# Performance work log

Hardware: AMD Instinct MI355X
Metric: run time of the kernel (lower is better)

The kernel has to match this reference:

```python
import jax, jax.numpy as jnp
import numpy as np

TEMP = 10.0  # self.temp in the module


def _l2norm(x, eps):
    # matches torch cosine_similarity / F.normalize eps-clamped L2 normalization
    n = jnp.sqrt(jnp.sum(x * x, axis=-1, keepdims=True))
    return x / jnp.maximum(n, eps)


def setup_inputs() -> dict:
    key = jax.random.key(0)
    k1, k2, k3, k4 = jax.random.split(key, 4)
    b, n, k, q, t, c = 2, 5, 5, 75, 196, 384  # 5-way 5-shot, 15 queries/way, ViT-S tokens
    return {
        "feat_shot": jax.random.normal(k1, (b, n, k, t, c), jnp.float32),
        "feat_query": jax.random.normal(k2, (b, q, t, c), jnp.float32),
        "x_shot": jax.random.normal(k3, (b, n, k, c), jnp.float32),
        "x_query": jax.random.normal(k4, (b, q, c), jnp.float32),
    }


def reference(feat_shot, feat_query, x_shot, x_query):
    b, n, k, t, c = feat_shot.shape
    # --- token-level cosine similarity branch ---
    fq = _l2norm(feat_query, 1e-8)                      # [b,q,t,c]
    fs = _l2norm(feat_shot.reshape(b, n, k * t, c), 1e-8)  # [b,n,k*t,c]
    # cosine sim of every query token vs every shot token of each class
    sim = jnp.einsum('bqtc,bnsc->bqnts', fq, fs)        # [b,q,n,t,k*t]
    # topk(k=1) over shot tokens -> max; .mean(-1) over the size-1 topk dim is identity;
    # then mean over query tokens t
    logits = jnp.max(sim, axis=-1).mean(axis=-1)        # [b,q,n]
    # --- global-feature classifier branch ---
    proto = _l2norm(x_shot.mean(axis=-2), 1e-12)        # prototype mean over k shots: [b,n,c]
    xq = _l2norm(x_query, 1e-12)                        # [b,q,c]
    cls_logits = TEMP * jnp.einsum('bqc,bnc->bqn', xq, proto)  # [b,q,n]
    return (logits, cls_logits)
```

## Files before the change

kernel.cpp:

```cpp
#include <hip/hip_runtime.h>
#include <hip/hip_bf16.h>
#include <hip/hip_fp8.h>
#include <stdint.h>


typedef __attribute__((ext_vector_type(8))) int int8v;
typedef __attribute__((ext_vector_type(4))) float f32x4;

__device__ __forceinline__ unsigned enc_f(float f) {
    unsigned b = __float_as_uint(f);
    return (b & 0x80000000u) ? ~b : (b | 0x80000000u);
}
__device__ __forceinline__ float dec_f(unsigned u) {
    unsigned b = (u & 0x80000000u) ? (u & 0x7FFFFFFFu) : ~u;
    return __uint_as_float(b);
}

__device__ __forceinline__ unsigned pack4_fp8(float a, float b, float c, float d) {
    int r = __builtin_amdgcn_cvt_pk_fp8_f32(a, b, 0, false);
    r = __builtin_amdgcn_cvt_pk_fp8_f32(c, d, r, true);
    return (unsigned)r;
}

__global__ void prep_kernel(const float* __restrict__ feat_query,
                            const float* __restrict__ feat_shot,
                            const float* __restrict__ x_shot,
                            unsigned* __restrict__ fqn,
                            unsigned* __restrict__ fsnp,
                            float* __restrict__ proto,
                            unsigned* __restrict__ P) {
    const int blk  = blockIdx.x;
    const int tid  = threadIdx.x;
    const int lane = tid & 63;
    const int wv   = tid >> 6;

    if (blk < 2478) {
        const int tr  = blk * 16 + wv * 4 + (lane >> 4);
        const int l16 = lane & 15;
        if (tr >= 39640) return;

        const float* row;
        unsigned* o32;
        bool zero = false;
        bool shot = false;
        if (tr < 29400) {
            row = feat_query + (size_t)tr * 384;
            o32 = fqn + (size_t)tr * 96;
        } else {
            const int sp = tr - 29400;
            const int bn = sp >> 10;
            const int s  = sp & 1023;
            row  = feat_shot + ((size_t)bn * 980 + s) * 384;
            zero = (s >= 980);
            shot = true;
            const int shh   = s >> 9;
            const int c     = s & 511;
            const int chunk = c >> 5;
            const int cl    = c & 31;
            o32 = fsnp + (size_t)bn * 98304 + shh * 49152 + chunk * 3072
                       + (cl >> 4) * 512 + (cl & 15) * 4;
        }
        int idxs[6];
#pragma unroll
        for (int j = 0; j < 6; ++j)
            idxs[j] = shot ? ((j >> 1) * 1024 + ((l16 >> 2) & 1) * 256
                              + (((j & 1) << 1) + (l16 >> 3)) * 64 + (l16 & 3))
                           : (l16 + 16 * j);

        if (zero) {
#pragma unroll
            for (int j = 0; j < 6; ++j) o32[idxs[j]] = 0u;
            return;
        }
        const float4* rf4 = (const float4*)row;
        float4 v[6];
        float ss = 0.f;
#pragma unroll
        for (int j = 0; j < 6; ++j) {
            v[j] = rf4[l16 + 16 * j];
            ss += v[j].x * v[j].x + v[j].y * v[j].y + v[j].z * v[j].z + v[j].w * v[j].w;
        }
#pragma unroll
        for (int off = 1; off < 16; off <<= 1) ss += __shfl_xor(ss, off, 64);
        const float sc = 1.0f / fmaxf(sqrtf(ss), 1e-8f);
#pragma unroll
        for (int j = 0; j < 6; ++j)
            o32[idxs[j]] = pack4_fp8(v[j].x * sc, v[j].y * sc, v[j].z * sc, v[j].w * sc);
    } else if (blk < 2481) {
        const int gw = (blk - 2478) * 4 + wv;
        if (gw >= 10) return;
        const float* base = x_shot + (size_t)gw * 5 * 384;
        float v[6];
        float ss = 0.f;
#pragma unroll
        for (int j = 0; j < 6; ++j) {
            float s = 0.f;
#pragma unroll
            for (int kk = 0; kk < 5; ++kk) s += base[kk * 384 + lane + 64 * j];
            s *= 0.2f;
            v[j] = s;
            ss += s * s;
        }
#pragma unroll
        for (int off = 1; off < 64; off <<= 1) ss += __shfl_xor(ss, off, 64);
        const float scale = 1.0f / fmaxf(sqrtf(ss), 1e-12f);
#pragma unroll
        for (int j = 0; j < 6; ++j) proto[(size_t)gw * 384 + lane + 64 * j] = v[j] * scale;
    } else {
        const int i = (blk - 2481) * 256 + tid;
        if (i < 147000) P[i] = 0u;
    }
}

__global__ __launch_bounds__(256, 2) void gemm_kernel(const uint8_t* __restrict__ fqn,
                                                      const uint8_t* __restrict__ fsnp,
                                                      unsigned* __restrict__ P) {
    const int p   = blockIdx.x;
    const int w   = (p & 7) * 145 + (p >> 3);
    const int b   = w / 580;
    const int rem = w - b * 580;
    const int mt  = rem / 10;
    const int g   = rem - mt * 10;
    const int sh  = g & 1;
    const int bc  = b * 5 + (g >> 1);
    const int m0  = mt * 256;

    const int tid  = threadIdx.x;
    const int lane = tid & 63;
    const int wv   = tid >> 6;
    const int l15  = lane & 15;
    const int hi   = lane >> 4;

    const uint8_t* Ag = fqn  + (size_t)b * 14700 * 384;
    const uint8_t* Bg = fsnp + (size_t)bc * 393216 + (size_t)sh * 196608;
    const uint8_t* bp = Bg + lane * 16;

    int8v A[4][3];
#pragma unroll
    for (int mi = 0; mi < 4; ++mi) {
        int row = m0 + wv * 64 + mi * 16 + l15;
        row = row < 14700 ? row : 14699;
        const uint8_t* pa = Ag + (size_t)row * 384 + hi * 32;
#pragma unroll
        for (int ks = 0; ks < 3; ++ks) {
            const uint4 x = *(const uint4*)(pa + ks * 128);
            const uint4 y = *(const uint4*)(pa + ks * 128 + 16);
            A[mi][ks] = (int8v){(int)x.x, (int)x.y, (int)x.z, (int)x.w,
                                (int)y.x, (int)y.y, (int)y.z, (int)y.w};
        }
    }

    float rmax[4][4];
#pragma unroll
    for (int mi = 0; mi < 4; ++mi)
#pragma unroll
        for (int i = 0; i < 4; ++i) rmax[mi][i] = -3.0e38f;

    uint4 S[3][4];
#pragma unroll
    for (int ks = 0; ks < 3; ++ks) {
        const uint8_t* p2 = bp + (size_t)ks * 4096;
#pragma unroll
        for (int j = 0; j < 4; ++j)
            S[ks][j] = *(const uint4*)(p2 + j * 1024);
    }

    for (int chunk = 0; chunk < 16; ++chunk) {
        f32x4 acc[4][2];
#pragma unroll
        for (int mi = 0; mi < 4; ++mi)
#pragma unroll
            for (int nf = 0; nf < 2; ++nf) acc[mi][nf] = (f32x4){0.f, 0.f, 0.f, 0.f};

#pragma unroll
        for (int ks = 0; ks < 3; ++ks) {
            const int8v Bf0 = (int8v){(int)S[ks][0].x, (int)S[ks][0].y,
                                      (int)S[ks][0].z, (int)S[ks][0].w,
                                      (int)S[ks][1].x, (int)S[ks][1].y,
                                      (int)S[ks][1].z, (int)S[ks][1].w};
            const int8v Bf1 = (int8v){(int)S[ks][2].x, (int)S[ks][2].y,
                                      (int)S[ks][2].z, (int)S[ks][2].w,
                                      (int)S[ks][3].x, (int)S[ks][3].y,
                                      (int)S[ks][3].z, (int)S[ks][3].w};
#pragma unroll
            for (int mi = 0; mi < 4; ++mi) {
                acc[mi][0] = __builtin_amdgcn_mfma_scale_f32_16x16x128_f8f6f4(
                    A[mi][ks], Bf0, acc[mi][0],
                    0, 0, 0, 0x7F7F7F7F, 0, 0x7F7F7F7F);
                acc[mi][1] = __builtin_amdgcn_mfma_scale_f32_16x16x128_f8f6f4(
                    A[mi][ks], Bf1, acc[mi][1],
                    0, 0, 0, 0x7F7F7F7F, 0, 0x7F7F7F7F);
            }
            {
                const int kn = chunk * 3 + ks + 3;
                const int kc = kn < 48 ? kn : 47;
                const uint8_t* p2 = bp + (size_t)kc * 4096;
#pragma unroll
                for (int j = 0; j < 4; ++j)
                    S[ks][j] = *(const uint4*)(p2 + j * 1024);
            }
        }

#pragma unroll
        for (int nf = 0; nf < 2; ++nf) {
            if (sh * 512 + chunk * 32 + nf * 16 + l15 < 980) {
#pragma unroll
                for (int mi = 0; mi < 4; ++mi)
#pragma unroll
                    for (int i = 0; i < 4; ++i)
                        rmax[mi][i] = fmaxf(rmax[mi][i], acc[mi][nf][i]);
            }
        }
    }

#pragma unroll
    for (int mi = 0; mi < 4; ++mi)
#pragma unroll
        for (int i = 0; i < 4; ++i) {
            float v = rmax[mi][i];
#pragma unroll
            for (int off = 1; off < 16; off <<= 1) v = fmaxf(v, __shfl_xor(v, off, 64));
            if (l15 == 0) {
                const int row = m0 + wv * 64 + mi * 16 + hi * 4 + i;
                if (row < 14700)
                    atomicMax(&P[(size_t)bc * 14700 + row], enc_f(v));
            }
        }
}

__global__ void final_kernel(const unsigned* __restrict__ P,
                             const float* __restrict__ xq,
                             const float* __restrict__ proto,
                             float* __restrict__ out) {
    const int blk  = blockIdx.x;
    const int tid  = threadIdx.x;
    const int lane = tid & 63;
    const int wv   = tid >> 6;

    if (blk < 188) {
        const int gw = blk * 4 + wv;
        if (gw >= 750) return;
        const int n  = gw % 5;
        const int bq = gw / 5;
        const int b  = bq / 75;
        const int q  = bq % 75;
        const unsigned* row = P + (size_t)(b * 5 + n) * 14700 + q * 196;
        float s = 0.f;
        for (int t = lane; t < 196; t += 64) s += dec_f(row[t]);
#pragma unroll
        for (int off = 1; off < 64; off <<= 1) s += __shfl_xor(s, off, 64);
        if (lane == 0) out[gw] = s * (1.0f / 196.0f);
    } else {
        const int gw = (blk - 188) * 4 + wv;
        if (gw >= 150) return;
        const float* row = xq + (size_t)gw * 384;
        float u[6];
        float ss = 0.f;
#pragma unroll
        for (int j = 0; j < 6; ++j) { u[j] = row[lane + 64 * j]; ss += u[j] * u[j]; }
#pragma unroll
        for (int off = 1; off < 64; off <<= 1) ss += __shfl_xor(ss, off, 64);
        const float scale = 1.0f / fmaxf(sqrtf(ss), 1e-12f);
#pragma unroll
        for (int j = 0; j < 6; ++j) u[j] *= scale;
        const int b = gw / 75;
        for (int n = 0; n < 5; ++n) {
            const float* p = proto + (size_t)(b * 5 + n) * 384;
            float d = 0.f;
#pragma unroll
            for (int j = 0; j < 6; ++j) d += u[j] * p[lane + 64 * j];
#pragma unroll
            for (int off = 1; off < 64; off <<= 1) d += __shfl_xor(d, off, 64);
            if (lane == 0) out[750 + gw * 5 + n] = 10.0f * d;
        }
    }
}

extern "C" void kernel_launch(void* const* d_in, const int* in_sizes, int n_in,
                              void* d_out, int out_size, void* d_ws, size_t ws_size,
                              hipStream_t stream) {
    const float* feat_shot  = (const float*)d_in[0];
    const float* feat_query = (const float*)d_in[1];
    const float* x_shot     = (const float*)d_in[2];
    const float* x_query    = (const float*)d_in[3];
    float* out = (float*)d_out;
    char* ws = (char*)d_ws;

    uint8_t*  fqn   = (uint8_t*)ws;
    uint8_t*  fsnp  = (uint8_t*)(ws + 11289600);
    float*    proto = (float*)(ws + 15221760);
    unsigned* P     = (unsigned*)(ws + 15237120);

    prep_kernel<<<3056, 256, 0, stream>>>(feat_query, feat_shot, x_shot,
                                          (unsigned*)fqn, (unsigned*)fsnp, proto, P);
    gemm_kernel<<<1160, 256, 0, stream>>>(fqn, fsnp, P);
    final_kernel<<<226, 256, 0, stream>>>(P, x_query, proto, out);
}
```

Baseline: 151.9 us.

## Shrink GEMM row tile to 192 and double-buffer B prefetch for higher occupancy

The M tile per block drops from 256 to 192 rows (48 per wave), which cuts A-fragment and accumulator registers and raises launch bounds to 3 blocks per SM. The B prefetch ring shrinks from three slots to two, with the loop unrolled over two chunks. Grid size and the XCD-aware block remap are recomputed for 1540 blocks. The trade-off is more blocks, more B traffic per row computed and more atomics, plus a shorter prefetch distance that could expose load latency.

```diff
diff --git a/kernel.cpp b/kernel.cpp
--- a/kernel.cpp
+++ b/kernel.cpp
@@ -112,18 +112,20 @@
     }
 }
 
-__global__ __launch_bounds__(256, 2) void gemm_kernel(const uint8_t* __restrict__ fqn,
+__global__ __launch_bounds__(256, 3) void gemm_kernel(const uint8_t* __restrict__ fqn,
                                                       const uint8_t* __restrict__ fsnp,
                                                       unsigned* __restrict__ P) {
     const int p   = blockIdx.x;
-    const int w   = (p & 7) * 145 + (p >> 3);
-    const int b   = w / 580;
-    const int rem = w - b * 580;
+    const int c   = p & 7;
+    const int pos = p >> 3;
+    const int w   = (c < 4 ? c * 193 : 772 + (c - 4) * 192) + pos;
+    const int b   = w / 770;
+    const int rem = w - b * 770;
     const int mt  = rem / 10;
     const int g   = rem - mt * 10;
     const int sh  = g & 1;
     const int bc  = b * 5 + (g >> 1);
-    const int m0  = mt * 256;
+    const int m0  = mt * 192;
 
     const int tid  = threadIdx.x;
     const int lane = tid & 63;
@@ -135,10 +137,10 @@
     const uint8_t* Bg = fsnp + (size_t)bc * 393216 + (size_t)sh * 196608;
     const uint8_t* bp = Bg + lane * 16;
 
-    int8v A[4][3];
-#pragma unroll
-    for (int mi = 0; mi < 4; ++mi) {
-        int row = m0 + wv * 64 + mi * 16 + l15;
+    int8v A[3][3];
+#pragma unroll
+    for (int mi = 0; mi < 3; ++mi) {
+        int row = m0 + wv * 48 + mi * 16 + l15;
         row = row < 14700 ? row : 14699;
         const uint8_t* pa = Ag + (size_t)row * 384 + hi * 32;
 #pragma unroll
@@ -150,40 +152,43 @@
         }
     }
 
-    float rmax[4][4];
-#pragma unroll
-    for (int mi = 0; mi < 4; ++mi)
+    float rmax[3][4];
+#pragma unroll
+    for (int mi = 0; mi < 3; ++mi)
 #pragma unroll
         for (int i = 0; i < 4; ++i) rmax[mi][i] = -3.0e38f;
 
-    uint4 S[3][4];
-#pragma unroll
-    for (int ks = 0; ks < 3; ++ks) {
-        const uint8_t* p2 = bp + (size_t)ks * 4096;
+    uint4 S[2][4];
+#pragma unroll
+    for (int sl = 0; sl < 2; ++sl) {
+        const uint8_t* p2 = bp + (size_t)sl * 4096;
 #pragma unroll
         for (int j = 0; j < 4; ++j)
-            S[ks][j] = *(const uint4*)(p2 + j * 1024);
-    }
-
-    for (int chunk = 0; chunk < 16; ++chunk) {
-        f32x4 acc[4][2];
-#pragma unroll
-        for (int mi = 0; mi < 4; ++mi)
+            S[sl][j] = *(const uint4*)(p2 + j * 1024);
+    }
+
+    for (int cp = 0; cp < 8; ++cp) {
+        f32x4 acc[3][2];
+#pragma unroll
+        for (int mi = 0; mi < 3; ++mi)
 #pragma unroll
             for (int nf = 0; nf < 2; ++nf) acc[mi][nf] = (f32x4){0.f, 0.f, 0.f, 0.f};
 
 #pragma unroll
-        for (int ks = 0; ks < 3; ++ks) {
-            const int8v Bf0 = (int8v){(int)S[ks][0].x, (int)S[ks][0].y,
-                                      (int)S[ks][0].z, (int)S[ks][0].w,
-                                      (int)S[ks][1].x, (int)S[ks][1].y,
-                                      (int)S[ks][1].z, (int)S[ks][1].w};
-            const int8v Bf1 = (int8v){(int)S[ks][2].x, (int)S[ks][2].y,
-                                      (int)S[ks][2].z, (int)S[ks][2].w,
-                                      (int)S[ks][3].x, (int)S[ks][3].y,
-                                      (int)S[ks][3].z, (int)S[ks][3].w};
-#pragma unroll
-            for (int mi = 0; mi < 4; ++mi) {
+        for (int u = 0; u < 6; ++u) {
+            constexpr int SLOT_LUT[6] = {0, 1, 0, 1, 0, 1};
+            const int sl = SLOT_LUT[u];
+            const int8v Bf0 = (int8v){(int)S[sl][0].x, (int)S[sl][0].y,
+                                      (int)S[sl][0].z, (int)S[sl][0].w,
+                                      (int)S[sl][1].x, (int)S[sl][1].y,
+                                      (int)S[sl][1].z, (int)S[sl][1].w};
+            const int8v Bf1 = (int8v){(int)S[sl][2].x, (int)S[sl][2].y,
+                                      (int)S[sl][2].z, (int)S[sl][2].w,
+                                      (int)S[sl][3].x, (int)S[sl][3].y,
+                                      (int)S[sl][3].z, (int)S[sl][3].w};
+            const int ks = (u < 3) ? u : u - 3;
+#pragma unroll
+            for (int mi = 0; mi < 3; ++mi) {
                 acc[mi][0] = __builtin_amdgcn_mfma_scale_f32_16x16x128_f8f6f4(
                     A[mi][ks], Bf0, acc[mi][0],
                     0, 0, 0, 0x7F7F7F7F, 0, 0x7F7F7F7F);
@@ -192,36 +197,45 @@
                     0, 0, 0, 0x7F7F7F7F, 0, 0x7F7F7F7F);
             }
             {
-                const int kn = chunk * 3 + ks + 3;
+                const int kn = cp * 6 + u + 2;
                 const int kc = kn < 48 ? kn : 47;
                 const uint8_t* p2 = bp + (size_t)kc * 4096;
 #pragma unroll
                 for (int j = 0; j < 4; ++j)
-                    S[ks][j] = *(const uint4*)(p2 + j * 1024);
+                    S[sl][j] = *(const uint4*)(p2 + j * 1024);
             }
-        }
-
-#pragma unroll
-        for (int nf = 0; nf < 2; ++nf) {
-            if (sh * 512 + chunk * 32 + nf * 16 + l15 < 980) {
-#pragma unroll
-                for (int mi = 0; mi < 4; ++mi)
-#pragma unroll
-                    for (int i = 0; i < 4; ++i)
-                        rmax[mi][i] = fmaxf(rmax[mi][i], acc[mi][nf][i]);
+            if (u == 2 || u == 5) {
+                const int ch = cp * 2 + (u == 5 ? 1 : 0);
+#pragma unroll
+                for (int nf = 0; nf < 2; ++nf) {
+                    if (sh * 512 + ch * 32 + nf * 16 + l15 < 980) {
+#pragma unroll
+                        for (int mi = 0; mi < 3; ++mi)
+#pragma unroll
+                            for (int i = 0; i < 4; ++i)
+                                rmax[mi][i] = fmaxf(rmax[mi][i], acc[mi][nf][i]);
+                    }
+                }
+                if (u == 2) {
+#pragma unroll
+                    for (int mi = 0; mi < 3; ++mi)
+#pragma unroll
+                        for (int nf = 0; nf < 2; ++nf)
+                            acc[mi][nf] = (f32x4){0.f, 0.f, 0.f, 0.f};
+                }
             }
         }
     }
 
 #pragma unroll
-    for (int mi = 0; mi < 4; ++mi)
+    for (int mi = 0; mi < 3; ++mi)
 #pragma unroll
         for (int i = 0; i < 4; ++i) {
             float v = rmax[mi][i];
 #pragma unroll
             for (int off = 1; off < 16; off <<= 1) v = fmaxf(v, __shfl_xor(v, off, 64));
             if (l15 == 0) {
-                const int row = m0 + wv * 64 + mi * 16 + hi * 4 + i;
+                const int row = m0 + wv * 48 + mi * 16 + hi * 4 + i;
                 if (row < 14700)
                     atomicMax(&P[(size_t)bc * 14700 + row], enc_f(v));
             }
@@ -293,6 +307,6 @@
 
     prep_kernel<<<3056, 256, 0, stream>>>(feat_query, feat_shot, x_shot,
                                           (unsigned*)fqn, (unsigned*)fsnp, proto, P);
-    gemm_kernel<<<1160, 256, 0, stream>>>(fqn, fsnp, P);
+    gemm_kernel<<<1540, 256, 0, stream>>>(fqn, fsnp, P);
     final_kernel<<<226, 256, 0, stream>>>(P, x_query, proto, out);
 }
```

After: 216.0 us. 1.42x slower.

## Fuse final reduction into GEMM, drop shot-half split and atomicMax buffer

Applied to the files above, without the earlier changes.

Each GEMM block now covers all 980 shot tokens of its class instead of half, so the max is complete in registers and the per-row atomicMax into a workspace buffer goes away. The mean over query tokens is done in the GEMM epilogue by summing row maxima per query and atomically adding into the output. The global classifier branch runs in extra blocks of the GEMM launch, and the final kernel and the large zero-fill are removed. The cost is fewer, longer blocks (580 instead of 1160), which may reduce parallelism and latency hiding, and float atomicAdd ordering makes the sums nondeterministic.

```diff
diff --git a/kernel.cpp b/kernel.cpp
--- a/kernel.cpp
+++ b/kernel.cpp
@@ -6,15 +6,6 @@
 
 typedef __attribute__((ext_vector_type(8))) int int8v;
 typedef __attribute__((ext_vector_type(4))) float f32x4;
-
-__device__ __forceinline__ unsigned enc_f(float f) {
-    unsigned b = __float_as_uint(f);
-    return (b & 0x80000000u) ? ~b : (b | 0x80000000u);
-}
-__device__ __forceinline__ float dec_f(unsigned u) {
-    unsigned b = (u & 0x80000000u) ? (u & 0x7FFFFFFFu) : ~u;
-    return __uint_as_float(b);
-}
 
 __device__ __forceinline__ unsigned pack4_fp8(float a, float b, float c, float d) {
     int r = __builtin_amdgcn_cvt_pk_fp8_f32(a, b, 0, false);
@@ -28,7 +19,7 @@
                             unsigned* __restrict__ fqn,
                             unsigned* __restrict__ fsnp,
                             float* __restrict__ proto,
-                            unsigned* __restrict__ P) {
+                            float* __restrict__ out) {
     const int blk  = blockIdx.x;
     const int tid  = threadIdx.x;
     const int lane = tid & 63;
@@ -107,22 +98,54 @@
 #pragma unroll
         for (int j = 0; j < 6; ++j) proto[(size_t)gw * 384 + lane + 64 * j] = v[j] * scale;
     } else {
-        const int i = (blk - 2481) * 256 + tid;
-        if (i < 147000) P[i] = 0u;
+        for (int i = tid; i < 750; i += 256) out[i] = 0.f;
     }
 }
 
 __global__ __launch_bounds__(256, 2) void gemm_kernel(const uint8_t* __restrict__ fqn,
                                                       const uint8_t* __restrict__ fsnp,
-                                                      unsigned* __restrict__ P) {
-    const int p   = blockIdx.x;
-    const int w   = (p & 7) * 145 + (p >> 3);
-    const int b   = w / 580;
-    const int rem = w - b * 580;
-    const int mt  = rem / 10;
-    const int g   = rem - mt * 10;
-    const int sh  = g & 1;
-    const int bc  = b * 5 + (g >> 1);
+                                                      const float* __restrict__ xq,
+                                                      const float* __restrict__ proto,
+                                                      float* __restrict__ out) {
+    const int p = blockIdx.x;
+
+    if (p >= 580) {
+        const int tid  = threadIdx.x;
+        const int lane = tid & 63;
+        const int wv   = tid >> 6;
+        const int gw   = (p - 580) * 4 + wv;
+        if (gw >= 150) return;
+        const float* row = xq + (size_t)gw * 384;
+        float u[6];
+        float ss = 0.f;
+#pragma unroll
+        for (int j = 0; j < 6; ++j) { u[j] = row[lane + 64 * j]; ss += u[j] * u[j]; }
+#pragma unroll
+        for (int off = 1; off < 64; off <<= 1) ss += __shfl_xor(ss, off, 64);
+        const float scale = 1.0f / fmaxf(sqrtf(ss), 1e-12f);
+#pragma unroll
+        for (int j = 0; j < 6; ++j) u[j] *= scale;
+        const int b = gw / 75;
+        for (int n = 0; n < 5; ++n) {
+            const float* pr = proto + (size_t)(b * 5 + n) * 384;
+            float d = 0.f;
+#pragma unroll
+            for (int j = 0; j < 6; ++j) d += u[j] * pr[lane + 64 * j];
+#pragma unroll
+            for (int off = 1; off < 64; off <<= 1) d += __shfl_xor(d, off, 64);
+            if (lane == 0) out[750 + gw * 5 + n] = 10.0f * d;
+        }
+        return;
+    }
+
+    const int c   = p & 7;
+    const int pos = p >> 3;
+    const int w   = (c < 4 ? c * 73 : 292 + (c - 4) * 72) + pos;
+    const int b   = w / 290;
+    const int rem = w - b * 290;
+    const int mt  = rem / 5;
+    const int cls = rem - mt * 5;
+    const int bc  = b * 5 + cls;
     const int m0  = mt * 256;
 
     const int tid  = threadIdx.x;
@@ -132,7 +155,7 @@
     const int hi   = lane >> 4;
 
     const uint8_t* Ag = fqn  + (size_t)b * 14700 * 384;
-    const uint8_t* Bg = fsnp + (size_t)bc * 393216 + (size_t)sh * 196608;
+    const uint8_t* Bg = fsnp + (size_t)bc * 393216;
     const uint8_t* bp = Bg + lane * 16;
 
     int8v A[4][3];
@@ -165,7 +188,7 @@
             S[ks][j] = *(const uint4*)(p2 + j * 1024);
     }
 
-    for (int chunk = 0; chunk < 16; ++chunk) {
+    for (int chunk = 0; chunk < 31; ++chunk) {
         f32x4 acc[4][2];
 #pragma unroll
         for (int mi = 0; mi < 4; ++mi)
@@ -193,7 +216,7 @@
             }
             {
                 const int kn = chunk * 3 + ks + 3;
-                const int kc = kn < 48 ? kn : 47;
+                const int kc = kn < 93 ? kn : 92;
                 const uint8_t* p2 = bp + (size_t)kc * 4096;
 #pragma unroll
                 for (int j = 0; j < 4; ++j)
@@ -203,7 +226,7 @@
 
 #pragma unroll
         for (int nf = 0; nf < 2; ++nf) {
-            if (sh * 512 + chunk * 32 + nf * 16 + l15 < 980) {
+            if (chunk * 32 + nf * 16 + l15 < 980) {
 #pragma unroll
                 for (int mi = 0; mi < 4; ++mi)
 #pragma unroll
@@ -213,6 +236,9 @@
         }
     }
 
+    const int start = m0 + wv * 64;
+    const int qbase = start / 196;
+    float a0 = 0.f, a1 = 0.f;
 #pragma unroll
     for (int mi = 0; mi < 4; ++mi)
 #pragma unroll
@@ -221,58 +247,17 @@
 #pragma unroll
             for (int off = 1; off < 16; off <<= 1) v = fmaxf(v, __shfl_xor(v, off, 64));
             if (l15 == 0) {
-                const int row = m0 + wv * 64 + mi * 16 + hi * 4 + i;
-                if (row < 14700)
-                    atomicMax(&P[(size_t)bc * 14700 + row], enc_f(v));
-            }
-        }
-}
-
-__global__ void final_kernel(const unsigned* __restrict__ P,
-                             const float* __restrict__ xq,
-                             const float* __restrict__ proto,
-                             float* __restrict__ out) {
-    const int blk  = blockIdx.x;
-    const int tid  = threadIdx.x;
-    const int lane = tid & 63;
-    const int wv   = tid >> 6;
-
-    if (blk < 188) {
-        const int gw = blk * 4 + wv;
-        if (gw >= 750) return;
-        const int n  = gw % 5;
-        const int bq = gw / 5;
-        const int b  = bq / 75;
-        const int q  = bq % 75;
-        const unsigned* row = P + (size_t)(b * 5 + n) * 14700 + q * 196;
-        float s = 0.f;
-        for (int t = lane; t < 196; t += 64) s += dec_f(row[t]);
-#pragma unroll
-        for (int off = 1; off < 64; off <<= 1) s += __shfl_xor(s, off, 64);
-        if (lane == 0) out[gw] = s * (1.0f / 196.0f);
-    } else {
-        const int gw = (blk - 188) * 4 + wv;
-        if (gw >= 150) return;
-        const float* row = xq + (size_t)gw * 384;
-        float u[6];
-        float ss = 0.f;
-#pragma unroll
-        for (int j = 0; j < 6; ++j) { u[j] = row[lane + 64 * j]; ss += u[j] * u[j]; }
-#pragma unroll
-        for (int off = 1; off < 64; off <<= 1) ss += __shfl_xor(ss, off, 64);
-        const float scale = 1.0f / fmaxf(sqrtf(ss), 1e-12f);
-#pragma unroll
-        for (int j = 0; j < 6; ++j) u[j] *= scale;
-        const int b = gw / 75;
-        for (int n = 0; n < 5; ++n) {
-            const float* p = proto + (size_t)(b * 5 + n) * 384;
-            float d = 0.f;
-#pragma unroll
-            for (int j = 0; j < 6; ++j) d += u[j] * p[lane + 64 * j];
-#pragma unroll
-            for (int off = 1; off < 64; off <<= 1) d += __shfl_xor(d, off, 64);
-            if (lane == 0) out[750 + gw * 5 + n] = 10.0f * d;
-        }
+                const int row = start + mi * 16 + hi * 4 + i;
+                if (row < 14700) {
+                    if (row / 196 == qbase) a0 += v; else a1 += v;
+                }
+            }
+        }
+    if (l15 == 0 && start < 14700) {
+        atomicAdd(&out[(b * 75 + qbase) * 5 + cls], a0 * (1.0f / 196.0f));
+        const int rend = start + 63 < 14699 ? start + 63 : 14699;
+        if (rend / 196 != qbase)
+            atomicAdd(&out[(b * 75 + qbase + 1) * 5 + cls], a1 * (1.0f / 196.0f));
     }
 }
 
@@ -289,10 +274,8 @@
     uint8_t*  fqn   = (uint8_t*)ws;
     uint8_t*  fsnp  = (uint8_t*)(ws + 11289600);
     float*    proto = (float*)(ws + 15221760);
-    unsigned* P     = (unsigned*)(ws + 15237120);
-
-    prep_kernel<<<3056, 256, 0, stream>>>(feat_query, feat_shot, x_shot,
-                                          (unsigned*)fqn, (unsigned*)fsnp, proto, P);
-    gemm_kernel<<<1160, 256, 0, stream>>>(fqn, fsnp, P);
-    final_kernel<<<226, 256, 0, stream>>>(P, x_query, proto, out);
-}
+
+    prep_kernel<<<2482, 256, 0, stream>>>(feat_query, feat_shot, x_shot,
+                                          (unsigned*)fqn, (unsigned*)fsnp, proto, out);
+    gemm_kernel<<<618, 256, 0, stream>>>(fqn, fsnp, x_query, proto, out);
+}
```

Result: no change. 153.8 us (+1.3%).
